# Performance work log

Measured on AMD Instinct MI355X. Metric: run time of the kernel, lower is better.

Reference implementation:

```python
import math
import jax, jax.numpy as jnp
import numpy as np

B, H, T, D = 1, 4, 1024, 8192  # D = 128 * 256 // 4 (hardcoded module constants)
THETA = 2.0 ** 16


def _frequency(d):
    # quantize(arange(d)) = floor(t/2)*2 ; freq = 1/theta**(q/d)/(2*pi)
    t = jnp.arange(d, dtype=jnp.float32)
    q = jnp.floor(t / 2.0) * 2.0
    return 1.0 / (THETA ** (q / d)) / (2.0 * math.pi)  # [D]


def _rope(v):
    # Faithful to original: slices dim 1 (heads), then row-major reshape back.
    v_rot = jnp.stack([-v[:, 1::2], v[:, ::2]], axis=-1).reshape(v.shape)
    freq = _frequency(v.shape[-1])  # [D]
    phases = jnp.arange(v.shape[2], dtype=jnp.float32)[:, None] * freq[None, :]  # [T, D]
    phases = (phases % 1.0) * (2.0 * math.pi)
    cos = jnp.cos(phases)[None, None]  # [1,1,T,D]
    sin = jnp.sin(phases)[None, None]
    return (v * cos).astype(v.dtype) + (v_rot * sin).astype(v.dtype)


def setup_inputs() -> dict:
    key = jax.random.key(0)
    k1, k2 = jax.random.split(key)
    query = jax.random.normal(k1, (B, H, T, D), dtype=jnp.float32)
    value = jax.random.normal(k2, (B, H, T, D), dtype=jnp.float32)
    return {"query": query, "value": value}


def reference(query, value):
    # key is query (asserted in original)
    q = _rope(query)  # [B,H,T,D]
    scale = 1.0 / math.sqrt(D)
    scores = jnp.einsum('bhtd,bhsd->bhts', q, q) * scale  # [B,H,T,T]
    t_idx = jnp.arange(T)
    causal = t_idx[:, None] > t_idx[None, :]  # tril(diagonal=-1): strictly lower
    scores = jnp.where(causal[None, None], scores, 0.0)
    return jnp.einsum('bhts,bhsd->bhtd', scores, value)
```

## Files before the change

kernel.cpp:

```cpp
#include <hip/hip_runtime.h>
#include <hip/hip_bf16.h>


typedef __bf16 bf16x8 __attribute__((ext_vector_type(8)));
typedef float  f32x4  __attribute__((ext_vector_type(4)));

#define HEAD_STRIDE (1024ull * 8192ull)

__device__ inline void gl_lds16(const void* g, void* l) {
  __builtin_amdgcn_global_load_lds(
      (__attribute__((address_space(1))) void*)(g),
      (__attribute__((address_space(3))) void*)(l), 16, 0, 0);
}

__global__ __launch_bounds__(256) void rope_kernel(const float* __restrict__ Q,
                                                   __bf16* __restrict__ Qr) {
  int gid = blockIdx.x * 256 + threadIdx.x;
  size_t e8 = (size_t)gid * 8;
  int d0 = (int)(e8 & 8191);
  int t  = (int)((e8 >> 13) & 1023);
  int h  = (int)(e8 >> 23);

  f32x4 qa = *(const f32x4*)(Q + e8);
  f32x4 qb = *(const f32x4*)(Q + e8 + 4);
  int pt   = t & 1;
  int srct = ((h & 1) << 9) + (t >> 1);
  int sd   = (d0 >> 1) + (pt << 12);
  int hh   = h & ~1;
  size_t soff = ((size_t)srct << 13) + (size_t)sd;
  f32x4 a4 = *(const f32x4*)(Q + (size_t)(hh + 1) * HEAD_STRIDE + soff);
  f32x4 b4 = *(const f32x4*)(Q + (size_t)hh       * HEAD_STRIDE + soff);

  float qv[8];
#pragma unroll
  for (int i = 0; i < 4; ++i) { qv[i] = qa[i]; qv[4 + i] = qb[i]; }

  bf16x8 o;
  float tf = (float)t;
#pragma unroll
  for (int p = 0; p < 4; ++p) {
    float qd = (float)(d0 + 2 * p);
    float fr = exp2f(-qd * (1.0f / 512.0f)) * 0.15915494309189535f;
    float x = tf * fr;
    x -= floorf(x);
    float sn, cs;
    __sincosf(x * 6.283185307179586f, &sn, &cs);
    o[2 * p]     = (__bf16)(qv[2 * p]     * cs - a4[p] * sn);
    o[2 * p + 1] = (__bf16)(qv[2 * p + 1] * cs + b4[p] * sn);
  }
  *(bf16x8*)(Qr + e8) = o;
}

__global__ __launch_bounds__(256) void s1_qqt(const __bf16* __restrict__ Qr,
                                              __bf16* __restrict__ Sbf,
                                              __bf16* __restrict__ part) {
  __shared__ __align__(16) __bf16 As[128 * 64];
  __shared__ __align__(16) __bf16 Bs[128 * 64];
  int bid = blockIdx.x;
  int x = bid & 7;
  int g = bid >> 3;
  int hi = (g >= 36) ? 1 : 0;
  int pair = g - 36 * hi;
  int c = x * 2 + hi;
  int h = c >> 2, split = c & 3;
  int ti = 0, p = pair;
  while (p > ti) { p -= ti + 1; ++ti; }
  int si = p;

  const __bf16* Abase = Qr + (size_t)h * HEAD_STRIDE + ((size_t)(ti * 128) << 13) + split * 2048;
  const __bf16* Bbase = Qr + (size_t)h * HEAD_STRIDE + ((size_t)(si * 128) << 13) + split * 2048;

  int tid = threadIdx.x, lane = tid & 63, wave = tid >> 6;
  int wm = (wave & 1) << 6, wn = (wave >> 1) << 6;
  int l16 = lane & 15, q4 = lane >> 4;
  int srow = lane >> 3;
  int scol = ((lane & 7) ^ srow) * 8;

  f32x4 acc[4][4] = {};

  for (int kk = 0; kk < 2048; kk += 64) {
#pragma unroll
    for (int j = 0; j < 4; ++j) {
      int cc = wave * 4 + j;
      int row = cc * 8 + srow;
      gl_lds16(Abase + (size_t)row * 8192 + kk + scol, &As[cc * 512]);
      gl_lds16(Bbase + (size_t)row * 8192 + kk + scol, &Bs[cc * 512]);
    }
    __syncthreads();
#pragma unroll
    for (int ks = 0; ks < 64; ks += 32) {
      bf16x8 af[4], bfr[4];
#pragma unroll
      for (int i = 0; i < 4; ++i) {
        int r = wm + i * 16 + l16;
        af[i] = *(const bf16x8*)&As[r * 64 + (((q4 + (ks >> 3)) ^ (r & 7)) << 3)];
      }
#pragma unroll
      for (int i = 0; i < 4; ++i) {
        int r = wn + i * 16 + l16;
        bfr[i] = *(const bf16x8*)&Bs[r * 64 + (((q4 + (ks >> 3)) ^ (r & 7)) << 3)];
      }
#pragma unroll
      for (int i = 0; i < 4; ++i)
#pragma unroll
        for (int j = 0; j < 4; ++j)
          acc[i][j] = __builtin_amdgcn_mfma_f32_16x16x32_bf16(af[i], bfr[j], acc[i][j], 0, 0, 0);
    }
    __syncthreads();
  }

  const float scale = 0.011048543456039806f;
  if (split == 0) {
    __bf16* Sh = Sbf + ((size_t)h << 20);
    int t_base = ti * 128 + wm, s_base = si * 128 + wn;
#pragma unroll
    for (int i = 0; i < 4; ++i)
#pragma unroll
      for (int j = 0; j < 4; ++j) {
        int col = s_base + j * 16 + l16;
#pragma unroll
        for (int r = 0; r < 4; ++r) {
          int row = t_base + i * 16 + q4 * 4 + r;
          Sh[((size_t)row << 10) + col] = (__bf16)(acc[i][j][r] * scale);
        }
      }
  } else {
    __bf16* P = part + (((size_t)(h * 36 + pair) * 3 + (split - 1)) << 14);
#pragma unroll
    for (int i = 0; i < 4; ++i)
#pragma unroll
      for (int j = 0; j < 4; ++j) {
        int lcol = wn + j * 16 + l16;
#pragma unroll
        for (int r = 0; r < 4; ++r) {
          int lrow = wm + i * 16 + q4 * 4 + r;
          P[lrow * 128 + lcol] = (__bf16)(acc[i][j][r] * scale);
        }
      }
  }
}

__global__ __launch_bounds__(256) void reduce_kernel(const __bf16* __restrict__ part,
                                                     __bf16* __restrict__ Sbf) {
  int gid = blockIdx.x * 256 + threadIdx.x;
  int tile = gid >> 11;
  int e = (gid & 2047) << 3;
  int row = e >> 7, col = e & 127;
  int h = tile / 36, pair = tile % 36;
  int ti = 0, p = pair;
  while (p > ti) { p -= ti + 1; ++ti; }
  int si = p;

  size_t soff = ((size_t)h << 20) + ((size_t)(ti * 128 + row) << 10) + si * 128 + col;
  bf16x8 s0 = *(const bf16x8*)(Sbf + soff);
  const __bf16* P = part + ((size_t)tile * 3 << 14) + row * 128 + col;
  bf16x8 p0 = *(const bf16x8*)(P);
  bf16x8 p1 = *(const bf16x8*)(P + 16384);
  bf16x8 p2 = *(const bf16x8*)(P + 32768);
  bool diag = (ti == si);
  bf16x8 o;
#pragma unroll
  for (int j = 0; j < 8; ++j) {
    float v = (float)s0[j] + (float)p0[j] + (float)p1[j] + (float)p2[j];
    if (diag && (col + j >= row)) v = 0.0f;
    o[j] = (__bf16)v;
  }
  *(bf16x8*)(Sbf + soff) = o;
}

__global__ __launch_bounds__(256) void transp_kernel(const float* __restrict__ V,
                                                     __bf16* __restrict__ Vt) {
  __shared__ __bf16 L[64 * 72];
  int bid = blockIdx.x;
  int dtile = bid & 127;
  int st = (bid >> 7) & 15;
  int h = bid >> 11;
  int s0 = st << 6, d0 = dtile << 6;
  const float* Vh = V + (size_t)h * HEAD_STRIDE;
  __bf16* Vth = Vt + (size_t)h * HEAD_STRIDE;
  int tid = threadIdx.x;
  int r = tid >> 2;
  int c = (tid & 3) << 4;
#pragma unroll
  for (int j = 0; j < 4; ++j) {
    f32x4 v = *(const f32x4*)(Vh + (size_t)(s0 + r) * 8192 + d0 + c + 4 * j);
#pragma unroll
    for (int e = 0; e < 4; ++e) L[(c + 4 * j + e) * 72 + r] = (__bf16)v[e];
  }
  __syncthreads();
  int row = tid >> 3;
  int col8 = (tid & 7) << 3;
#pragma unroll
  for (int half = 0; half < 2; ++half) {
    int dr = row + half * 32;
    bf16x8 v = *(const bf16x8*)&L[dr * 72 + col8];
    *(bf16x8*)(Vth + (size_t)(d0 + dr) * 1024 + s0 + col8) = v;
  }
}

__global__ __launch_bounds__(256) void s3_sv(const __bf16* __restrict__ Sbf,
                                             const __bf16* __restrict__ Vt,
                                             float* __restrict__ out) {
  __shared__ __align__(16) __bf16 As[128 * 64];
  __shared__ __align__(16) __bf16 Bs[128 * 64];
  int bid = blockIdx.x;
  int dt = bid & 63; bid >>= 6;
  int tt = 7 - (bid & 7);
  int h = bid >> 3;

  const __bf16* Abase = Sbf + ((size_t)h << 20) + ((size_t)(tt * 128) << 10);
  const __bf16* Bbase = Vt + (size_t)h * HEAD_STRIDE + ((size_t)(dt * 128) << 10);
  int Kmax = tt * 128 + 128;

  int tid = threadIdx.x, lane = tid & 63, wave = tid >> 6;
  int wm = (wave & 1) << 6, wn = (wave >> 1) << 6;
  int l16 = lane & 15, q4 = lane >> 4;
  int srow = lane >> 3;
  int scol = ((lane & 7) ^ srow) * 8;

  f32x4 acc[4][4] = {};

  for (int kk = 0; kk < Kmax; kk += 64) {
#pragma unroll
    for (int j = 0; j < 4; ++j) {
      int cc = wave * 4 + j;
      int row = cc * 8 + srow;
      gl_lds16(Abase + (size_t)row * 1024 + kk + scol, &As[cc * 512]);
      gl_lds16(Bbase + (size_t)row * 1024 + kk + scol, &Bs[cc * 512]);
    }
    __syncthreads();
#pragma unroll
    for (int ks = 0; ks < 64; ks += 32) {
      bf16x8 af[4], bfr[4];
#pragma unroll
      for (int i = 0; i < 4; ++i) {
        int r = wm + i * 16 + l16;
        af[i] = *(const bf16x8*)&As[r * 64 + (((q4 + (ks >> 3)) ^ (r & 7)) << 3)];
      }
#pragma unroll
      for (int i = 0; i < 4; ++i) {
        int r = wn + i * 16 + l16;
        bfr[i] = *(const bf16x8*)&Bs[r * 64 + (((q4 + (ks >> 3)) ^ (r & 7)) << 3)];
      }
#pragma unroll
      for (int i = 0; i < 4; ++i)
#pragma unroll
        for (int j = 0; j < 4; ++j)
          acc[i][j] = __builtin_amdgcn_mfma_f32_16x16x32_bf16(af[i], bfr[j], acc[i][j], 0, 0, 0);
    }
    __syncthreads();
  }

  int t_base = tt * 128 + wm, d_base = dt * 128 + wn;
  float* obase = out + (size_t)h * HEAD_STRIDE;
#pragma unroll
  for (int i = 0; i < 4; ++i)
#pragma unroll
    for (int j = 0; j < 4; ++j) {
      int col = d_base + j * 16 + l16;
#pragma unroll
      for (int r = 0; r < 4; ++r) {
        int row = t_base + i * 16 + q4 * 4 + r;
        obase[((size_t)row << 13) + col] = acc[i][j][r];
      }
    }
}

extern "C" void kernel_launch(void* const* d_in, const int* in_sizes, int n_in,
                              void* d_out, int out_size, void* d_ws, size_t ws_size,
                              hipStream_t stream) {
  const float* query = (const float*)d_in[0];
  const float* value = (const float*)d_in[1];
  float* out = (float*)d_out;

  char* ws = (char*)d_ws;
  __bf16* Qr   = (__bf16*)ws;
  __bf16* Vt   = (__bf16*)ws;
  __bf16* Sbf  = (__bf16*)(ws + 67108864);
  __bf16* part = (__bf16*)(ws + 75497472);

  hipMemsetAsync(Sbf, 0, 8388608, stream);
  rope_kernel<<<16384, 256, 0, stream>>>(query, Qr);
  s1_qqt<<<576, 256, 0, stream>>>(Qr, Sbf, part);
  reduce_kernel<<<1152, 256, 0, stream>>>(part, Sbf);
  transp_kernel<<<8192, 256, 0, stream>>>(value, Vt);
  s3_sv<<<2048, 256, 0, stream>>>(Sbf, Vt, out);
}
```

Baseline: 453.0 us.

## Double-buffer LDS tiles in QK^T and SV GEMM kernels

Both MFMA GEMM kernels (s1_qqt and s3_sv) now use two LDS buffers per operand. Each iteration issues the global-to-LDS loads for the next K tile before running the MFMA work on the current tile, so memory latency overlaps with compute. This also drops one barrier per iteration. In exchange, LDS use per block doubles to 64KB, which can cut the number of resident blocks per CU and reduce latency hiding across blocks.

Result: no change. 446.0 us (-1.5%).

```diff
diff --git a/kernel.cpp b/kernel.cpp
--- a/kernel.cpp
+++ b/kernel.cpp
@@ -54,8 +54,8 @@
 __global__ __launch_bounds__(256) void s1_qqt(const __bf16* __restrict__ Qr,
                                               __bf16* __restrict__ Sbf,
                                               __bf16* __restrict__ part) {
-  __shared__ __align__(16) __bf16 As[128 * 64];
-  __shared__ __align__(16) __bf16 Bs[128 * 64];
+  __shared__ __align__(16) __bf16 As[2][128 * 64];
+  __shared__ __align__(16) __bf16 Bs[2][128 * 64];
   int bid = blockIdx.x;
   int x = bid & 7;
   int g = bid >> 3;
@@ -76,29 +76,36 @@
   int srow = lane >> 3;
   int scol = ((lane & 7) ^ srow) * 8;
 
-  f32x4 acc[4][4] = {};
-
-  for (int kk = 0; kk < 2048; kk += 64) {
+  auto stage = [&](int b, int kk) {
 #pragma unroll
     for (int j = 0; j < 4; ++j) {
       int cc = wave * 4 + j;
       int row = cc * 8 + srow;
-      gl_lds16(Abase + (size_t)row * 8192 + kk + scol, &As[cc * 512]);
-      gl_lds16(Bbase + (size_t)row * 8192 + kk + scol, &Bs[cc * 512]);
-    }
-    __syncthreads();
+      gl_lds16(Abase + (size_t)row * 8192 + kk + scol, &As[b][cc * 512]);
+      gl_lds16(Bbase + (size_t)row * 8192 + kk + scol, &Bs[b][cc * 512]);
+    }
+  };
+
+  f32x4 acc[4][4] = {};
+
+  stage(0, 0);
+  __syncthreads();
+
+  int cur = 0;
+  for (int kk = 0; kk < 2048; kk += 64) {
+    if (kk + 64 < 2048) stage(cur ^ 1, kk + 64);
 #pragma unroll
     for (int ks = 0; ks < 64; ks += 32) {
       bf16x8 af[4], bfr[4];
 #pragma unroll
       for (int i = 0; i < 4; ++i) {
         int r = wm + i * 16 + l16;
-        af[i] = *(const bf16x8*)&As[r * 64 + (((q4 + (ks >> 3)) ^ (r & 7)) << 3)];
+        af[i] = *(const bf16x8*)&As[cur][r * 64 + (((q4 + (ks >> 3)) ^ (r & 7)) << 3)];
       }
 #pragma unroll
       for (int i = 0; i < 4; ++i) {
         int r = wn + i * 16 + l16;
-        bfr[i] = *(const bf16x8*)&Bs[r * 64 + (((q4 + (ks >> 3)) ^ (r & 7)) << 3)];
+        bfr[i] = *(const bf16x8*)&Bs[cur][r * 64 + (((q4 + (ks >> 3)) ^ (r & 7)) << 3)];
       }
 #pragma unroll
       for (int i = 0; i < 4; ++i)
@@ -107,6 +114,7 @@
           acc[i][j] = __builtin_amdgcn_mfma_f32_16x16x32_bf16(af[i], bfr[j], acc[i][j], 0, 0, 0);
     }
     __syncthreads();
+    cur ^= 1;
   }
 
   const float scale = 0.011048543456039806f;
@@ -201,8 +209,8 @@
 __global__ __launch_bounds__(256) void s3_sv(const __bf16* __restrict__ Sbf,
                                              const __bf16* __restrict__ Vt,
                                              float* __restrict__ out) {
-  __shared__ __align__(16) __bf16 As[128 * 64];
-  __shared__ __align__(16) __bf16 Bs[128 * 64];
+  __shared__ __align__(16) __bf16 As[2][128 * 64];
+  __shared__ __align__(16) __bf16 Bs[2][128 * 64];
   int bid = blockIdx.x;
   int dt = bid & 63; bid >>= 6;
   int tt = 7 - (bid & 7);
@@ -218,29 +226,36 @@
   int srow = lane >> 3;
   int scol = ((lane & 7) ^ srow) * 8;
 
-  f32x4 acc[4][4] = {};
-
-  for (int kk = 0; kk < Kmax; kk += 64) {
+  auto stage = [&](int b, int kk) {
 #pragma unroll
     for (int j = 0; j < 4; ++j) {
       int cc = wave * 4 + j;
       int row = cc * 8 + srow;
-      gl_lds16(Abase + (size_t)row * 1024 + kk + scol, &As[cc * 512]);
-      gl_lds16(Bbase + (size_t)row * 1024 + kk + scol, &Bs[cc * 512]);
-    }
-    __syncthreads();
+      gl_lds16(Abase + (size_t)row * 1024 + kk + scol, &As[b][cc * 512]);
+      gl_lds16(Bbase + (size_t)row * 1024 + kk + scol, &Bs[b][cc * 512]);
+    }
+  };
+
+  f32x4 acc[4][4] = {};
+
+  stage(0, 0);
+  __syncthreads();
+
+  int cur = 0;
+  for (int kk = 0; kk < Kmax; kk += 64) {
+    if (kk + 64 < Kmax) stage(cur ^ 1, kk + 64);
 #pragma unroll
     for (int ks = 0; ks < 64; ks += 32) {
       bf16x8 af[4], bfr[4];
 #pragma unroll
       for (int i = 0; i < 4; ++i) {
         int r = wm + i * 16 + l16;
-        af[i] = *(const bf16x8*)&As[r * 64 + (((q4 + (ks >> 3)) ^ (r & 7)) << 3)];
+        af[i] = *(const bf16x8*)&As[cur][r * 64 + (((q4 + (ks >> 3)) ^ (r & 7)) << 3)];
       }
 #pragma unroll
       for (int i = 0; i < 4; ++i) {
         int r = wn + i * 16 + l16;
-        bfr[i] = *(const bf16x8*)&Bs[r * 64 + (((q4 + (ks >> 3)) ^ (r & 7)) << 3)];
+        bfr[i] = *(const bf16x8*)&Bs[cur][r * 64 + (((q4 + (ks >> 3)) ^ (r & 7)) << 3)];
       }
 #pragma unroll
       for (int i = 0; i < 4; ++i)
@@ -249,6 +264,7 @@
           acc[i][j] = __builtin_amdgcn_mfma_f32_16x16x32_bf16(af[i], bfr[j], acc[i][j], 0, 0, 0);
     }
     __syncthreads();
+    cur ^= 1;
   }
 
   int t_base = tt * 128 + wm, d_base = dt * 128 + wn;
```
